# Optimization experiments

Hardware: AMD Instinct MI355X
Metric: run time of the kernel (lower is better)

The kernel has to match this reference:

```python
import jax, jax.numpy as jnp
import numpy as np

N = 50000      # nodes
E = 800000     # edges
D_IN = 128
D_H = 128      # dim_h
D_OUT = 1
G = 64         # graphs in batch


def _glorot(key, fan_in, fan_out):
    return jax.random.normal(key, (fan_in, fan_out), jnp.float32) / np.sqrt(fan_in)


def setup_inputs() -> dict:
    key = jax.random.key(0)
    ks = jax.random.split(key, 12)
    x = jax.random.normal(ks[0], (N, D_IN), jnp.float32)
    edge_index = jax.random.randint(ks[1], (2, E), 0, N, dtype=jnp.int32)
    batch = jnp.sort(jax.random.randint(ks[2], (N,), 0, G, dtype=jnp.int32))
    # SAGEConv params: lin_l (bias) on aggregated neighbors, lin_r (no bias) on root
    Wl1 = _glorot(ks[3], D_IN, 2 * D_H); bl1 = jnp.zeros((2 * D_H,), jnp.float32)
    Wr1 = _glorot(ks[4], D_IN, 2 * D_H)
    Wl2 = _glorot(ks[5], 2 * D_H, D_H); bl2 = jnp.zeros((D_H,), jnp.float32)
    Wr2 = _glorot(ks[6], 2 * D_H, D_H)
    Wl3 = _glorot(ks[7], D_H, 16); bl3 = jnp.zeros((16,), jnp.float32)
    Wr3 = _glorot(ks[8], D_H, 16)
    Wc = _glorot(ks[9], 16, D_OUT); bc = jnp.zeros((D_OUT,), jnp.float32)
    return dict(x=x, edge_index=edge_index, batch=batch,
                Wl1=Wl1, bl1=bl1, Wr1=Wr1,
                Wl2=Wl2, bl2=bl2, Wr2=Wr2,
                Wl3=Wl3, bl3=bl3, Wr3=Wr3,
                Wc=Wc, bc=bc)


def _segment_mean(vals, ids, num_segments):
    s = jax.ops.segment_sum(vals, ids, num_segments=num_segments)
    cnt = jax.ops.segment_sum(jnp.ones((vals.shape[0], 1), vals.dtype), ids,
                              num_segments=num_segments)
    return s / jnp.maximum(cnt, 1.0)


def _sage_conv(x, src, dst, Wl, bl, Wr):
    # PyG SAGEConv (mean aggr): lin_l(mean_{j in N(i)} x_j) + lin_r(x_i)
    mean_nbr = _segment_mean(x[src], dst, x.shape[0])  # gather + segment-mean
    return mean_nbr @ Wl + bl + x @ Wr


def reference(x, edge_index, batch,
              Wl1, bl1, Wr1, Wl2, bl2, Wr2, Wl3, bl3, Wr3, Wc, bc):
    src, dst = edge_index[0], edge_index[1]
    h = jax.nn.relu(_sage_conv(x, src, dst, Wl1, bl1, Wr1))   # [N, 256]
    # dropout p=0.5 skipped (training=False)
    h = jax.nn.relu(_sage_conv(h, src, dst, Wl2, bl2, Wr2))   # [N, 128]
    # dropout p=0.2 skipped (training=False)
    h = _sage_conv(h, src, dst, Wl3, bl3, Wr3)                # [N, 16]
    h_pool = _segment_mean(h, batch, G)                       # global_mean_pool [G,16]
    # final dropout is hardcoded training=True in source -> fixed-key dropout
    keep = jax.random.bernoulli(jax.random.key(42), 0.5, h_pool.shape)
    hd = jnp.where(keep, h_pool * 2.0, 0.0)
    out = (hd @ Wc + bc).reshape(-1)                          # [G*dim_out]
    return out, h_pool
```

## Files before the change

kernel.cpp:

```cpp
#include <hip/hip_runtime.h>
#include <stdint.h>


#define GG 64
#define NXCD 8
#define BCAP 112000

typedef __attribute__((ext_vector_type(8))) unsigned short ushort8;
typedef __attribute__((ext_vector_type(8))) short bf16s8;
typedef __attribute__((ext_vector_type(4))) float f32x4;

__device__ __forceinline__ unsigned short rne_bf16(float f) {
  unsigned u = __float_as_uint(f);
  return (unsigned short)((u + 0x7FFFu + ((u >> 16) & 1u)) >> 16);
}
__device__ __forceinline__ float bf2f(unsigned short b) {
  return __uint_as_float(((unsigned)b) << 16);
}

__global__ __launch_bounds__(256) void k_cvtprep(const float* __restrict__ x, unsigned short* __restrict__ xb,
                                                 int n8, int N,
                                                 const float* __restrict__ Wl1, const float* __restrict__ Wr1,
                                                 const float* __restrict__ Wl2, const float* __restrict__ Wr2,
                                                 const float* __restrict__ Wl3, const float* __restrict__ Wr3,
                                                 unsigned short* __restrict__ WT1l, unsigned short* __restrict__ WT1r,
                                                 unsigned short* __restrict__ WT2l, unsigned short* __restrict__ WT2r,
                                                 unsigned short* __restrict__ wc3b,
                                                 int* __restrict__ deg, int* __restrict__ bcur) {
  int idx = blockIdx.x * 256 + threadIdx.x;
  if (idx < n8) {
    const float4* p = (const float4*)(x + (size_t)idx * 8);
    float4 v0 = p[0], v1 = p[1];
    ushort8 o;
    o[0] = rne_bf16(v0.x); o[1] = rne_bf16(v0.y); o[2] = rne_bf16(v0.z); o[3] = rne_bf16(v0.w);
    o[4] = rne_bf16(v1.x); o[5] = rne_bf16(v1.y); o[6] = rne_bf16(v1.z); o[7] = rne_bf16(v1.w);
    *(ushort8*)(xb + (size_t)idx * 8) = o;
    return;
  }
  int j = idx - n8;
  if (j < 32768) {
    int k = j >> 8, m = j & 255;
    WT1l[m * 128 + k] = rne_bf16(Wl1[j]);
    WT1r[m * 128 + k] = rne_bf16(Wr1[j]);
  } else if (j < 65536) {
    int q = j - 32768;
    int k = q >> 7, m = q & 127;
    WT2l[m * 256 + k] = rne_bf16(Wl2[q]);
    WT2r[m * 256 + k] = rne_bf16(Wr2[q]);
  } else if (j < 69632) {
    int q = j - 65536;
    int m = q >> 7, k = q & 127;
    float v = (m < 16) ? Wl3[k * 16 + m] : Wr3[k * 16 + (m - 16)];
    wc3b[q] = rne_bf16(v);
  } else if (j < 69632 + N) {
    deg[j - 69632] = 0;
  } else if (j < 69632 + N + NXCD) {
    bcur[j - 69632 - N] = 0;
  }
}

__global__ __launch_bounds__(256) void k_bucket(const int* __restrict__ src, const int* __restrict__ dst,
                                                int* __restrict__ deg, int* __restrict__ bcur,
                                                int2* __restrict__ bucket, int E, int binsz) {
  __shared__ int cnt[NXCD];
  __shared__ int base[NXCD];
  const int tid = threadIdx.x;
  if (tid < NXCD) cnt[tid] = 0;
  __syncthreads();
  int e0 = (blockIdx.x * 256 + tid) * 4;
  int d[4], s[4], bk[4], rk[4];
  int nv = 0;
  if (e0 + 3 < E) {
    int4 d4 = *(const int4*)(dst + e0);
    int4 s4 = *(const int4*)(src + e0);
    d[0] = d4.x; d[1] = d4.y; d[2] = d4.z; d[3] = d4.w;
    s[0] = s4.x; s[1] = s4.y; s[2] = s4.z; s[3] = s4.w;
    nv = 4;
  } else {
    for (int e = e0; e < E && nv < 4; ++e) { d[nv] = dst[e]; s[nv] = src[e]; ++nv; }
  }
#pragma unroll
  for (int k = 0; k < 4; ++k)
    if (k < nv) {
      atomicAdd(&deg[d[k]], 1);
      bk[k] = d[k] / binsz;
      rk[k] = atomicAdd(&cnt[bk[k]], 1);
    }
  __syncthreads();
  if (tid < NXCD) base[tid] = atomicAdd(&bcur[tid], cnt[tid]);
  __syncthreads();
#pragma unroll
  for (int k = 0; k < 4; ++k)
    if (k < nv) {
      int p = min(base[bk[k]] + rk[k], BCAP - 1);
      bucket[(size_t)bk[k] * BCAP + p] = make_int2(s[k], d[k]);
    }
}

__global__ __launch_bounds__(256) void k_scan_a(const int* __restrict__ deg, int* __restrict__ off,
                                                int* __restrict__ bsum, int N) {
  __shared__ int ws[256];
  const int tid = threadIdx.x;
  const int base = blockIdx.x * 1024 + tid * 4;
  int v0 = (base + 0 < N) ? deg[base + 0] : 0;
  int v1 = (base + 1 < N) ? deg[base + 1] : 0;
  int v2 = (base + 2 < N) ? deg[base + 2] : 0;
  int v3 = (base + 3 < N) ? deg[base + 3] : 0;
  int s = v0 + v1 + v2 + v3;
  ws[tid] = s;
  __syncthreads();
  for (int d = 1; d < 256; d <<= 1) {
    int t = (tid >= d) ? ws[tid - d] : 0;
    __syncthreads();
    ws[tid] += t;
    __syncthreads();
  }
  int excl = ws[tid] - s;
  if (tid == 255) bsum[blockIdx.x] = ws[255];
  if (base + 0 < N) off[base + 0] = excl;
  if (base + 1 < N) off[base + 1] = excl + v0;
  if (base + 2 < N) off[base + 2] = excl + v0 + v1;
  if (base + 3 < N) off[base + 3] = excl + v0 + v1 + v2;
}

__global__ __launch_bounds__(64) void k_scan_b(int* __restrict__ bsum, int nb) {
  int tid = threadIdx.x;
  int v = (tid < nb) ? bsum[tid] : 0;
  for (int d = 1; d < 64; d <<= 1) {
    int t = __shfl_up(v, d, 64);
    if (tid >= d) v += t;
  }
  if (tid < nb) bsum[tid] = v;
}

__global__ __launch_bounds__(256) void k_scan_c(int* __restrict__ off, int* __restrict__ cur,
                                                const int* __restrict__ bsum, int N, int nb) {
  int i = blockIdx.x * 256 + threadIdx.x;
  if (i < N) {
    int b = i >> 10;
    int v = off[i] + ((b > 0) ? bsum[b - 1] : 0);
    off[i] = v;
    cur[i] = v;
  }
  if (i == 0) off[N] = bsum[nb - 1];
}

__global__ __launch_bounds__(256) void k_fill2(const int2* __restrict__ bucket, const int* __restrict__ bcnt,
                                               const int* __restrict__ off, int* __restrict__ cur,
                                               int* __restrict__ eidx, int N, int binsz, int ngrp) {
  const int xcd = blockIdx.x & (NXCD - 1);
  const int grp = blockIdx.x >> 3;
  const int t = grp * 256 + threadIdx.x;
  const int nthr = ngrp * 256;
  const int lo = xcd * binsz;
  const int hi = min(lo + binsz, N);

  int s0 = off[lo] & ~15;
  int s1 = off[hi];
  for (int i = s0 + t * 16; i < s1; i += nthr * 16) {
    int v = eidx[i];
    asm volatile("" :: "v"(v));
  }

  const int cnt = min(bcnt[xcd], BCAP);
  const int2* seg = bucket + (size_t)xcd * BCAP;
  for (int e = t; e < cnt; e += nthr) {
    int2 sd = seg[e];
    int p = atomicAdd(&cur[sd.y], 1);
    eidx[p] = sd.x;
  }
}

template <int OUTBF>
__global__ __launch_bounds__(256) void k_aggr_b(const unsigned short* __restrict__ feat,
                                                const int* __restrict__ off, const int* __restrict__ eidx,
                                                void* __restrict__ out, int N) {
  int idx = blockIdx.x * 256 + threadIdx.x;
  int n = idx >> 4;
  if (n >= N) return;
  int c = (idx & 15) * 8;
  int b = off[n], e = off[n + 1];
  float s0 = 0.f, s1 = 0.f, s2 = 0.f, s3 = 0.f, s4 = 0.f, s5 = 0.f, s6 = 0.f, s7 = 0.f;
  int j = b;
  for (; j + 3 < e; j += 4) {
    int i0 = eidx[j], i1 = eidx[j + 1], i2 = eidx[j + 2], i3 = eidx[j + 3];
    ushort8 v0 = *(const ushort8*)&feat[(size_t)i0 * 128 + c];
    ushort8 v1 = *(const ushort8*)&feat[(size_t)i1 * 128 + c];
    ushort8 v2 = *(const ushort8*)&feat[(size_t)i2 * 128 + c];
    ushort8 v3 = *(const ushort8*)&feat[(size_t)i3 * 128 + c];
    s0 += bf2f(v0[0]) + bf2f(v1[0]) + bf2f(v2[0]) + bf2f(v3[0]);
    s1 += bf2f(v0[1]) + bf2f(v1[1]) + bf2f(v2[1]) + bf2f(v3[1]);
    s2 += bf2f(v0[2]) + bf2f(v1[2]) + bf2f(v2[2]) + bf2f(v3[2]);
    s3 += bf2f(v0[3]) + bf2f(v1[3]) + bf2f(v2[3]) + bf2f(v3[3]);
    s4 += bf2f(v0[4]) + bf2f(v1[4]) + bf2f(v2[4]) + bf2f(v3[4]);
    s5 += bf2f(v0[5]) + bf2f(v1[5]) + bf2f(v2[5]) + bf2f(v3[5]);
    s6 += bf2f(v0[6]) + bf2f(v1[6]) + bf2f(v2[6]) + bf2f(v3[6]);
    s7 += bf2f(v0[7]) + bf2f(v1[7]) + bf2f(v2[7]) + bf2f(v3[7]);
  }
  for (; j < e; ++j) {
    int sidx = eidx[j];
    ushort8 v = *(const ushort8*)&feat[(size_t)sidx * 128 + c];
    s0 += bf2f(v[0]); s1 += bf2f(v[1]); s2 += bf2f(v[2]); s3 += bf2f(v[3]);
    s4 += bf2f(v[4]); s5 += bf2f(v[5]); s6 += bf2f(v[6]); s7 += bf2f(v[7]);
  }
  float sc = 1.f / fmaxf((float)(e - b), 1.f);
  if (OUTBF) {
    ushort8 o;
    o[0] = rne_bf16(s0 * sc); o[1] = rne_bf16(s1 * sc); o[2] = rne_bf16(s2 * sc); o[3] = rne_bf16(s3 * sc);
    o[4] = rne_bf16(s4 * sc); o[5] = rne_bf16(s5 * sc); o[6] = rne_bf16(s6 * sc); o[7] = rne_bf16(s7 * sc);
    *(ushort8*)&((unsigned short*)out)[(size_t)n * 128 + c] = o;
  } else {
    float* po = &((float*)out)[(size_t)n * 128 + c];
    *(float4*)po = make_float4(s0 * sc, s1 * sc, s2 * sc, s3 * sc);
    *(float4*)(po + 4) = make_float4(s4 * sc, s5 * sc, s6 * sc, s7 * sc);
  }
}

template <int DUAL, int HAS_C0, int HAS_BIAS, int RELU, int OUT_BF16>
__global__ __launch_bounds__(256) void k_mgemm(
    const unsigned short* __restrict__ A1, int K1, const unsigned short* __restrict__ B1,
    const unsigned short* __restrict__ A2, const unsigned short* __restrict__ B2, int K2,
    const float* __restrict__ C0, const float* __restrict__ bias,
    void* __restrict__ Cout, int N, int M) {
  __shared__ unsigned short As[64 * 32];
  __shared__ unsigned short Bs[64 * 32];
  const int tid = threadIdx.x;
  const int row0 = blockIdx.y * 64;
  const int col0 = blockIdx.x * 64;
  const int lane = tid & 63;
  const int w = tid >> 6;
  const int wr = w >> 1, wc = w & 1;
  const int rl = lane & 15, g = lane >> 4;
  const int pos = ((g ^ ((rl >> 1) & 3)) << 3);
  const int srow = tid >> 2;
  const int schunk = tid & 3;
  const int spos = ((schunk ^ ((srow >> 1) & 3)) << 3);

  f32x4 acc00 = {0.f, 0.f, 0.f, 0.f}, acc01 = acc00, acc10 = acc00, acc11 = acc00;

  for (int pass = 0; pass < (DUAL ? 2 : 1); ++pass) {
    const unsigned short* __restrict__ A = pass ? A2 : A1;
    const unsigned short* __restrict__ B = pass ? B2 : B1;
    const int K = pass ? K2 : K1;
    for (int k0 = 0; k0 < K; k0 += 32) {
      {
        int r = row0 + srow;
        ushort8 va = (ushort8)(0);
        if (r < N) va = *(const ushort8*)&A[(size_t)r * K + k0 + schunk * 8];
        *(ushort8*)&As[srow * 32 + spos] = va;
        ushort8 vb = *(const ushort8*)&B[(size_t)(col0 + srow) * K + k0 + schunk * 8];
        *(ushort8*)&Bs[srow * 32 + spos] = vb;
      }
      __syncthreads();
      bf16s8 a0 = *(bf16s8*)&As[(wr * 32 + rl) * 32 + pos];
      bf16s8 a1 = *(bf16s8*)&As[(wr * 32 + 16 + rl) * 32 + pos];
      bf16s8 b0 = *(bf16s8*)&Bs[(wc * 32 + rl) * 32 + pos];
      bf16s8 b1 = *(bf16s8*)&Bs[(wc * 32 + 16 + rl) * 32 + pos];
      acc00 = __builtin_amdgcn_mfma_f32_16x16x32_bf16(a0, b0, acc00, 0, 0, 0);
      acc01 = __builtin_amdgcn_mfma_f32_16x16x32_bf16(a0, b1, acc01, 0, 0, 0);
      acc10 = __builtin_amdgcn_mfma_f32_16x16x32_bf16(a1, b0, acc10, 0, 0, 0);
      acc11 = __builtin_amdgcn_mfma_f32_16x16x32_bf16(a1, b1, acc11, 0, 0, 0);
      __syncthreads();
    }
  }

#pragma unroll
  for (int fi = 0; fi < 2; ++fi)
#pragma unroll
    for (int fj = 0; fj < 2; ++fj) {
      const f32x4 a = fi ? (fj ? acc11 : acc10) : (fj ? acc01 : acc00);
#pragma unroll
      for (int reg = 0; reg < 4; ++reg) {
        int r = row0 + wr * 32 + fi * 16 + g * 4 + reg;
        int c = col0 + wc * 32 + fj * 16 + rl;
        if (r >= N) continue;
        float v = a[reg];
        if (HAS_C0) v += C0[(size_t)r * M + c];
        if (HAS_BIAS) v += bias[c];
        if (RELU) v = fmaxf(v, 0.f);
        if (OUT_BF16) ((unsigned short*)Cout)[(size_t)r * M + c] = rne_bf16(v);
        else ((float*)Cout)[(size_t)r * M + c] = v;
      }
    }
}

__global__ __launch_bounds__(256) void k_mgemm3(const unsigned short* __restrict__ A,
                                                const unsigned short* __restrict__ B,
                                                float* __restrict__ C, int N) {
  __shared__ unsigned short As[128 * 32];
  __shared__ unsigned short Bs[32 * 32];
  const int tid = threadIdx.x;
  const int row0 = blockIdx.x * 128;
  const int lane = tid & 63;
  const int w = tid >> 6;
  const int rl = lane & 15, g = lane >> 4;
  const int pos = ((g ^ ((rl >> 1) & 3)) << 3);

  f32x4 acc00 = {0.f, 0.f, 0.f, 0.f}, acc01 = acc00, acc10 = acc00, acc11 = acc00;

  for (int k0 = 0; k0 < 128; k0 += 32) {
#pragma unroll
    for (int it = 0; it < 2; ++it) {
      int cid = tid + it * 256;
      int row = cid >> 2, ch = cid & 3;
      int r = row0 + row;
      ushort8 va = (ushort8)(0);
      if (r < N) va = *(const ushort8*)&A[(size_t)r * 128 + k0 + ch * 8];
      *(ushort8*)&As[row * 32 + ((ch ^ ((row >> 1) & 3)) << 3)] = va;
    }
    if (tid < 128) {
      int row = tid >> 2, ch = tid & 3;
      ushort8 vb = *(const ushort8*)&B[(size_t)row * 128 + k0 + ch * 8];
      *(ushort8*)&Bs[row * 32 + ((ch ^ ((row >> 1) & 3)) << 3)] = vb;
    }
    __syncthreads();
    bf16s8 a0 = *(bf16s8*)&As[(w * 32 + rl) * 32 + pos];
    bf16s8 a1 = *(bf16s8*)&As[(w * 32 + 16 + rl) * 32 + pos];
    bf16s8 b0 = *(bf16s8*)&Bs[rl * 32 + pos];
    bf16s8 b1 = *(bf16s8*)&Bs[(16 + rl) * 32 + pos];
    acc00 = __builtin_amdgcn_mfma_f32_16x16x32_bf16(a0, b0, acc00, 0, 0, 0);
    acc01 = __builtin_amdgcn_mfma_f32_16x16x32_bf16(a0, b1, acc01, 0, 0, 0);
    acc10 = __builtin_amdgcn_mfma_f32_16x16x32_bf16(a1, b0, acc10, 0, 0, 0);
    acc11 = __builtin_amdgcn_mfma_f32_16x16x32_bf16(a1, b1, acc11, 0, 0, 0);
    __syncthreads();
  }

#pragma unroll
  for (int fi = 0; fi < 2; ++fi)
#pragma unroll
    for (int fj = 0; fj < 2; ++fj) {
      const f32x4 a = fi ? (fj ? acc11 : acc10) : (fj ? acc01 : acc00);
#pragma unroll
      for (int reg = 0; reg < 4; ++reg) {
        int r = row0 + w * 32 + fi * 16 + g * 4 + reg;
        int c = fj * 16 + rl;
        if (r < N) C[(size_t)r * 32 + c] = a[reg];
      }
    }
}

__global__ __launch_bounds__(256) void k_l3post(const float* __restrict__ g3, const int* __restrict__ off,
                                                const int* __restrict__ eidx, const float* __restrict__ bl3,
                                                float* __restrict__ h3, int N) {
  int idx = blockIdx.x * 256 + threadIdx.x;
  int n = idx >> 2;
  if (n >= N) return;
  int c = (idx & 3) << 2;
  int b = off[n], e = off[n + 1];
  float ax = 0.f, ay = 0.f, az = 0.f, aw = 0.f;
  int j = b;
  for (; j + 3 < e; j += 4) {
    int i0 = eidx[j], i1 = eidx[j + 1], i2 = eidx[j + 2], i3 = eidx[j + 3];
    const float4 v0 = *(const float4*)&g3[(size_t)i0 * 32 + c];
    const float4 v1 = *(const float4*)&g3[(size_t)i1 * 32 + c];
    const float4 v2 = *(const float4*)&g3[(size_t)i2 * 32 + c];
    const float4 v3 = *(const float4*)&g3[(size_t)i3 * 32 + c];
    ax += v0.x + v1.x + v2.x + v3.x;
    ay += v0.y + v1.y + v2.y + v3.y;
    az += v0.z + v1.z + v2.z + v3.z;
    aw += v0.w + v1.w + v2.w + v3.w;
  }
  for (; j < e; ++j) {
    int s = eidx[j];
    const float4 v = *(const float4*)&g3[(size_t)s * 32 + c];
    ax += v.x; ay += v.y; az += v.z; aw += v.w;
  }
  float sc = 1.f / fmaxf((float)(e - b), 1.f);
  const float4 r2 = *(const float4*)&g3[(size_t)n * 32 + 16 + c];
  const float4 bb = *(const float4*)&bl3[c];
  *(float4*)&h3[(size_t)n * 16 + c] =
      make_float4(ax * sc + r2.x + bb.x, ay * sc + r2.y + bb.y,
                  az * sc + r2.z + bb.z, aw * sc + r2.w + bb.w);
}

__device__ __forceinline__ int lbound(const int* __restrict__ a, int n, int v) {
  int lo = 0, hi = n;
  while (lo < hi) {
    int mid = (lo + hi) >> 1;
    if (a[mid] < v) lo = mid + 1; else hi = mid;
  }
  return lo;
}

__global__ __launch_bounds__(256) void k_pool(const float* __restrict__ h3, const int* __restrict__ batch,
                                              int N, float* __restrict__ hpool, float* __restrict__ outp) {
  __shared__ float sm[4][16];
  int g = blockIdx.x, tid = threadIdx.x;
  int start = lbound(batch, N, g);
  int end = lbound(batch, N, g + 1);
  float acc[16];
#pragma unroll
  for (int j = 0; j < 16; ++j) acc[j] = 0.f;
  for (int i = start + tid; i < end; i += 256) {
    const float4* p = (const float4*)&h3[(size_t)i * 16];
    float4 v0 = p[0], v1 = p[1], v2 = p[2], v3 = p[3];
    acc[0] += v0.x; acc[1] += v0.y; acc[2] += v0.z; acc[3] += v0.w;
    acc[4] += v1.x; acc[5] += v1.y; acc[6] += v1.z; acc[7] += v1.w;
    acc[8] += v2.x; acc[9] += v2.y; acc[10] += v2.z; acc[11] += v2.w;
    acc[12] += v3.x; acc[13] += v3.y; acc[14] += v3.z; acc[15] += v3.w;
  }
#pragma unroll
  for (int j = 0; j < 16; ++j) {
    float v = acc[j];
    v += __shfl_down(v, 32);
    v += __shfl_down(v, 16);
    v += __shfl_down(v, 8);
    v += __shfl_down(v, 4);
    v += __shfl_down(v, 2);
    v += __shfl_down(v, 1);
    if ((tid & 63) == 0) sm[tid >> 6][j] = v;
  }
  __syncthreads();
  if (tid < 16) {
    float v = sm[0][tid] + sm[1][tid] + sm[2][tid] + sm[3][tid];
    v /= fmaxf((float)(end - start), 1.f);
    hpool[g * 16 + tid] = v;
    outp[g * 16 + tid] = v;
  }
}

__device__ __forceinline__ uint2 tf2x32(unsigned k0, unsigned k1, unsigned x0, unsigned x1) {
  const unsigned ks[3] = {k0, k1, k0 ^ k1 ^ 0x1BD11BDAu};
  const int rotA[4] = {13, 15, 26, 6}, rotB[4] = {17, 29, 16, 24};
  x0 += ks[0];
  x1 += ks[1];
#pragma unroll
  for (int i = 0; i < 5; ++i) {
    const int* R = (i & 1) ? rotB : rotA;
#pragma unroll
    for (int j = 0; j < 4; ++j) {
      x0 += x1;
      x1 = (x1 << R[j]) | (x1 >> (32 - R[j]));
      x1 ^= x0;
    }
    x0 += ks[(i + 1) % 3];
    x1 += ks[(i + 2) % 3] + (unsigned)(i + 1);
  }
  return make_uint2(x0, x1);
}

__global__ __launch_bounds__(1024) void k_final(const float* __restrict__ hpool,
                                                float* __restrict__ outp,
                                                const float* __restrict__ Wc,
                                                const float* __restrict__ bc) {
  int t = threadIdx.x;
  float m = hpool[t];
  uint2 r = tf2x32(0u, 42u, 0u, (unsigned)t);
  unsigned bits = r.x ^ r.y;
  float hd = (bits >> 31) ? 0.f : 2.f * m;
  float contrib = hd * Wc[t & 15];
  contrib += __shfl_down(contrib, 8, 16);
  contrib += __shfl_down(contrib, 4, 16);
  contrib += __shfl_down(contrib, 2, 16);
  contrib += __shfl_down(contrib, 1, 16);
  if ((t & 15) == 0) outp[t >> 4] = contrib + bc[0];
}

extern "C" void kernel_launch(void* const* d_in, const int* in_sizes, int n_in,
                              void* d_out, int out_size, void* d_ws, size_t ws_size,
                              hipStream_t stream) {
  const float* x   = (const float*)d_in[0];
  const int*   ei  = (const int*)d_in[1];
  const int*   bat = (const int*)d_in[2];
  const float* Wl1 = (const float*)d_in[3];
  const float* bl1 = (const float*)d_in[4];
  const float* Wr1 = (const float*)d_in[5];
  const float* Wl2 = (const float*)d_in[6];
  const float* bl2 = (const float*)d_in[7];
  const float* Wr2 = (const float*)d_in[8];
  const float* Wl3 = (const float*)d_in[9];
  const float* bl3 = (const float*)d_in[10];
  const float* Wr3 = (const float*)d_in[11];
  const float* Wc  = (const float*)d_in[12];
  const float* bc  = (const float*)d_in[13];

  const int E = in_sizes[1] / 2;
  const int N = in_sizes[2];
  const int* src = ei;
  const int* dst = ei + E;

  int*   off   = (int*)d_ws;
  int*   deg   = off + 50016;
  int*   bsum  = (int*)d_ws + 100016;
  int*   bcur  = (int*)d_ws + 100080;
  float* hpool = (float*)d_ws + 100096;
  unsigned short* wc3b = (unsigned short*)((float*)d_ws + 101120);
  unsigned short* WT1l = (unsigned short*)((float*)d_ws + 105216);
  unsigned short* WT1r = (unsigned short*)((float*)d_ws + 121600);
  unsigned short* WT2l = (unsigned short*)((float*)d_ws + 137984);
  unsigned short* WT2r = (unsigned short*)((float*)d_ws + 154368);
  int*   eidx  = (int*)d_ws + 170752;
  unsigned short* xb   = (unsigned short*)((float*)d_ws + 970752);
  unsigned short* aggb = (unsigned short*)((float*)d_ws + 4170752);
  unsigned short* h1b  = (unsigned short*)((float*)d_ws + 7370752);
  unsigned short* t2b  = xb;
  unsigned short* h2b  = (unsigned short*)((float*)d_ws + 970752);
  float* agg2 = (float*)d_ws + 13770752;
  int*   cur  = (int*)agg2;
  int2*  bucket = (int2*)((float*)d_ws + 13820800);
  float* g3   = (float*)d_ws + 7370752;
  float* h3   = (float*)d_ws + 8970752;
  float* outp = (float*)d_out;

  const int gy = (N + 63) / 64;
  const int gy3 = (N + 127) / 128;
  const int nb = (N + 1023) / 1024;
  const int n8 = N * 128 / 8;
  const int binsz = (N + NXCD - 1) / NXCD;
  const int ngrp = 64;

  const int prep_total = n8 + 69632 + N + NXCD;
  k_cvtprep<<<(prep_total + 255) / 256, 256, 0, stream>>>(x, xb, n8, N, Wl1, Wr1, Wl2, Wr2, Wl3, Wr3,
                                                          WT1l, WT1r, WT2l, WT2r, wc3b, deg, bcur);

  k_bucket<<<((E + 3) / 4 + 255) / 256, 256, 0, stream>>>(src, dst, deg, bcur, bucket, E, binsz);
  k_scan_a<<<nb, 256, 0, stream>>>(deg, off, bsum, N);
  k_scan_b<<<1, 64, 0, stream>>>(bsum, nb);
  k_scan_c<<<(N + 255) / 256, 256, 0, stream>>>(off, cur, bsum, N, nb);
  k_fill2<<<ngrp * NXCD, 256, 0, stream>>>(bucket, bcur, off, cur, eidx, N, binsz, ngrp);

  k_aggr_b<1><<<(N * 16 + 255) / 256, 256, 0, stream>>>(xb, off, eidx, aggb, N);
  k_mgemm<1, 0, 1, 1, 1><<<dim3(4, gy), 256, 0, stream>>>(aggb, 128, WT1l, xb, WT1r, 128,
                                                          nullptr, bl1, h1b, N, 256);

  k_mgemm<0, 0, 0, 0, 1><<<dim3(2, gy), 256, 0, stream>>>(h1b, 256, WT2l, nullptr, nullptr, 0,
                                                          nullptr, nullptr, t2b, N, 128);
  k_aggr_b<0><<<(N * 16 + 255) / 256, 256, 0, stream>>>(t2b, off, eidx, agg2, N);
  k_mgemm<0, 1, 1, 1, 1><<<dim3(2, gy), 256, 0, stream>>>(h1b, 256, WT2r, nullptr, nullptr, 0,
                                                          agg2, bl2, h2b, N, 128);

  k_mgemm3<<<gy3, 256, 0, stream>>>(h2b, wc3b, g3, N);
  k_l3post<<<(N * 4 + 255) / 256, 256, 0, stream>>>(g3, off, eidx, bl3, h3, N);

  k_pool<<<GG, 256, 0, stream>>>(h3, bat, N, hpool, outp + 64);
  k_final<<<1, 1024, 0, stream>>>(hpool, outp, Wc, bc);
}
```

Measured before the change: 241.8 us.

## Merge scan kernels, store layer-2 aggregate in bf16, fuse pool with final head

Replaces the three-kernel prefix scan with a single-block 1024-thread sequential-chunk scan. The layer-2 neighbour aggregate is now written as bf16 into the existing aggb buffer instead of fp32, halving that intermediate's traffic in both the aggregation and the GEMM epilogue. The pool and dropout/classifier kernels are fused into one, dropping a launch. Risks: the single-block scan walks about 49 chunks serially with many barriers, and bf16 rounding of the aggregate slightly reduces precision.

```diff
diff --git a/kernel.cpp b/kernel.cpp
--- a/kernel.cpp
+++ b/kernel.cpp
@@ -97,52 +97,32 @@
     }
 }
 
-__global__ __launch_bounds__(256) void k_scan_a(const int* __restrict__ deg, int* __restrict__ off,
-                                                int* __restrict__ bsum, int N) {
-  __shared__ int ws[256];
+__global__ __launch_bounds__(1024) void k_scan(const int* __restrict__ deg, int* __restrict__ off,
+                                               int* __restrict__ cur, int N) {
+  __shared__ int sm[1024];
   const int tid = threadIdx.x;
-  const int base = blockIdx.x * 1024 + tid * 4;
-  int v0 = (base + 0 < N) ? deg[base + 0] : 0;
-  int v1 = (base + 1 < N) ? deg[base + 1] : 0;
-  int v2 = (base + 2 < N) ? deg[base + 2] : 0;
-  int v3 = (base + 3 < N) ? deg[base + 3] : 0;
-  int s = v0 + v1 + v2 + v3;
-  ws[tid] = s;
-  __syncthreads();
-  for (int d = 1; d < 256; d <<= 1) {
-    int t = (tid >= d) ? ws[tid - d] : 0;
+  int running = 0;
+  for (int base = 0; base < N; base += 1024) {
+    int i = base + tid;
+    int v = (i < N) ? deg[i] : 0;
+    sm[tid] = v;
     __syncthreads();
-    ws[tid] += t;
+    for (int d = 1; d < 1024; d <<= 1) {
+      int t = (tid >= d) ? sm[tid - d] : 0;
+      __syncthreads();
+      sm[tid] += t;
+      __syncthreads();
+    }
+    if (i < N) {
+      int o = running + sm[tid] - v;
+      off[i] = o;
+      cur[i] = o;
+    }
+    int ct = sm[1023];
     __syncthreads();
-  }
-  int excl = ws[tid] - s;
-  if (tid == 255) bsum[blockIdx.x] = ws[255];
-  if (base + 0 < N) off[base + 0] = excl;
-  if (base + 1 < N) off[base + 1] = excl + v0;
-  if (base + 2 < N) off[base + 2] = excl + v0 + v1;
-  if (base + 3 < N) off[base + 3] = excl + v0 + v1 + v2;
-}
-
-__global__ __launch_bounds__(64) void k_scan_b(int* __restrict__ bsum, int nb) {
-  int tid = threadIdx.x;
-  int v = (tid < nb) ? bsum[tid] : 0;
-  for (int d = 1; d < 64; d <<= 1) {
-    int t = __shfl_up(v, d, 64);
-    if (tid >= d) v += t;
-  }
-  if (tid < nb) bsum[tid] = v;
-}
-
-__global__ __launch_bounds__(256) void k_scan_c(int* __restrict__ off, int* __restrict__ cur,
-                                                const int* __restrict__ bsum, int N, int nb) {
-  int i = blockIdx.x * 256 + threadIdx.x;
-  if (i < N) {
-    int b = i >> 10;
-    int v = off[i] + ((b > 0) ? bsum[b - 1] : 0);
-    off[i] = v;
-    cur[i] = v;
-  }
-  if (i == 0) off[N] = bsum[nb - 1];
+    running += ct;
+  }
+  if (tid == 0) off[N] = running;
 }
 
 __global__ __launch_bounds__(256) void k_fill2(const int2* __restrict__ bucket, const int* __restrict__ bcnt,
@@ -171,10 +151,9 @@
   }
 }
 
-template <int OUTBF>
 __global__ __launch_bounds__(256) void k_aggr_b(const unsigned short* __restrict__ feat,
                                                 const int* __restrict__ off, const int* __restrict__ eidx,
-                                                void* __restrict__ out, int N) {
+                                                unsigned short* __restrict__ out, int N) {
   int idx = blockIdx.x * 256 + threadIdx.x;
   int n = idx >> 4;
   if (n >= N) return;
@@ -204,23 +183,17 @@
     s4 += bf2f(v[4]); s5 += bf2f(v[5]); s6 += bf2f(v[6]); s7 += bf2f(v[7]);
   }
   float sc = 1.f / fmaxf((float)(e - b), 1.f);
-  if (OUTBF) {
-    ushort8 o;
-    o[0] = rne_bf16(s0 * sc); o[1] = rne_bf16(s1 * sc); o[2] = rne_bf16(s2 * sc); o[3] = rne_bf16(s3 * sc);
-    o[4] = rne_bf16(s4 * sc); o[5] = rne_bf16(s5 * sc); o[6] = rne_bf16(s6 * sc); o[7] = rne_bf16(s7 * sc);
-    *(ushort8*)&((unsigned short*)out)[(size_t)n * 128 + c] = o;
-  } else {
-    float* po = &((float*)out)[(size_t)n * 128 + c];
-    *(float4*)po = make_float4(s0 * sc, s1 * sc, s2 * sc, s3 * sc);
-    *(float4*)(po + 4) = make_float4(s4 * sc, s5 * sc, s6 * sc, s7 * sc);
-  }
+  ushort8 o;
+  o[0] = rne_bf16(s0 * sc); o[1] = rne_bf16(s1 * sc); o[2] = rne_bf16(s2 * sc); o[3] = rne_bf16(s3 * sc);
+  o[4] = rne_bf16(s4 * sc); o[5] = rne_bf16(s5 * sc); o[6] = rne_bf16(s6 * sc); o[7] = rne_bf16(s7 * sc);
+  *(ushort8*)&out[(size_t)n * 128 + c] = o;
 }
 
 template <int DUAL, int HAS_C0, int HAS_BIAS, int RELU, int OUT_BF16>
 __global__ __launch_bounds__(256) void k_mgemm(
     const unsigned short* __restrict__ A1, int K1, const unsigned short* __restrict__ B1,
     const unsigned short* __restrict__ A2, const unsigned short* __restrict__ B2, int K2,
-    const float* __restrict__ C0, const float* __restrict__ bias,
+    const unsigned short* __restrict__ C0, const float* __restrict__ bias,
     void* __restrict__ Cout, int N, int M) {
   __shared__ unsigned short As[64 * 32];
   __shared__ unsigned short Bs[64 * 32];
@@ -275,7 +248,7 @@
         int c = col0 + wc * 32 + fj * 16 + rl;
         if (r >= N) continue;
         float v = a[reg];
-        if (HAS_C0) v += C0[(size_t)r * M + c];
+        if (HAS_C0) v += bf2f(C0[(size_t)r * M + c]);
         if (HAS_BIAS) v += bias[c];
         if (RELU) v = fmaxf(v, 0.f);
         if (OUT_BF16) ((unsigned short*)Cout)[(size_t)r * M + c] = rne_bf16(v);
@@ -373,6 +346,26 @@
                   az * sc + r2.z + bb.z, aw * sc + r2.w + bb.w);
 }
 
+__device__ __forceinline__ uint2 tf2x32(unsigned k0, unsigned k1, unsigned x0, unsigned x1) {
+  const unsigned ks[3] = {k0, k1, k0 ^ k1 ^ 0x1BD11BDAu};
+  const int rotA[4] = {13, 15, 26, 6}, rotB[4] = {17, 29, 16, 24};
+  x0 += ks[0];
+  x1 += ks[1];
+#pragma unroll
+  for (int i = 0; i < 5; ++i) {
+    const int* R = (i & 1) ? rotB : rotA;
+#pragma unroll
+    for (int j = 0; j < 4; ++j) {
+      x0 += x1;
+      x1 = (x1 << R[j]) | (x1 >> (32 - R[j]));
+      x1 ^= x0;
+    }
+    x0 += ks[(i + 1) % 3];
+    x1 += ks[(i + 2) % 3] + (unsigned)(i + 1);
+  }
+  return make_uint2(x0, x1);
+}
+
 __device__ __forceinline__ int lbound(const int* __restrict__ a, int n, int v) {
   int lo = 0, hi = n;
   while (lo < hi) {
@@ -382,8 +375,9 @@
   return lo;
 }
 
-__global__ __launch_bounds__(256) void k_pool(const float* __restrict__ h3, const int* __restrict__ batch,
-                                              int N, float* __restrict__ hpool, float* __restrict__ outp) {
+__global__ __launch_bounds__(256) void k_poolfinal(const float* __restrict__ h3, const int* __restrict__ batch,
+                                                   int N, const float* __restrict__ Wc,
+                                                   const float* __restrict__ bc, float* __restrict__ outp) {
   __shared__ float sm[4][16];
   int g = blockIdx.x, tid = threadIdx.x;
   int start = lbound(batch, N, g);
@@ -414,46 +408,17 @@
   if (tid < 16) {
     float v = sm[0][tid] + sm[1][tid] + sm[2][tid] + sm[3][tid];
     v /= fmaxf((float)(end - start), 1.f);
-    hpool[g * 16 + tid] = v;
-    outp[g * 16 + tid] = v;
-  }
-}
-
-__device__ __forceinline__ uint2 tf2x32(unsigned k0, unsigned k1, unsigned x0, unsigned x1) {
-  const unsigned ks[3] = {k0, k1, k0 ^ k1 ^ 0x1BD11BDAu};
-  const int rotA[4] = {13, 15, 26, 6}, rotB[4] = {17, 29, 16, 24};
-  x0 += ks[0];
-  x1 += ks[1];
-#pragma unroll
-  for (int i = 0; i < 5; ++i) {
-    const int* R = (i & 1) ? rotB : rotA;
-#pragma unroll
-    for (int j = 0; j < 4; ++j) {
-      x0 += x1;
-      x1 = (x1 << R[j]) | (x1 >> (32 - R[j]));
-      x1 ^= x0;
-    }
-    x0 += ks[(i + 1) % 3];
-    x1 += ks[(i + 2) % 3] + (unsigned)(i + 1);
-  }
-  return make_uint2(x0, x1);
-}
-
-__global__ __launch_bounds__(1024) void k_final(const float* __restrict__ hpool,
-                                                float* __restrict__ outp,
-                                                const float* __restrict__ Wc,
-                                                const float* __restrict__ bc) {
-  int t = threadIdx.x;
-  float m = hpool[t];
-  uint2 r = tf2x32(0u, 42u, 0u, (unsigned)t);
-  unsigned bits = r.x ^ r.y;
-  float hd = (bits >> 31) ? 0.f : 2.f * m;
-  float contrib = hd * Wc[t & 15];
-  contrib += __shfl_down(contrib, 8, 16);
-  contrib += __shfl_down(contrib, 4, 16);
-  contrib += __shfl_down(contrib, 2, 16);
-  contrib += __shfl_down(contrib, 1, 16);
-  if ((t & 15) == 0) outp[t >> 4] = contrib + bc[0];
+    outp[64 + g * 16 + tid] = v;
+    uint2 r = tf2x32(0u, 42u, 0u, (unsigned)(g * 16 + tid));
+    unsigned bits = r.x ^ r.y;
+    float hd = (bits >> 31) ? 0.f : 2.f * v;
+    float contrib = hd * Wc[tid];
+    contrib += __shfl_down(contrib, 8, 16);
+    contrib += __shfl_down(contrib, 4, 16);
+    contrib += __shfl_down(contrib, 2, 16);
+    contrib += __shfl_down(contrib, 1, 16);
+    if (tid == 0) outp[g] = contrib + bc[0];
+  }
 }
 
 extern "C" void kernel_launch(void* const* d_in, const int* in_sizes, int n_in,
@@ -481,9 +446,7 @@
 
   int*   off   = (int*)d_ws;
   int*   deg   = off + 50016;
-  int*   bsum  = (int*)d_ws + 100016;
   int*   bcur  = (int*)d_ws + 100080;
-  float* hpool = (float*)d_ws + 100096;
   unsigned short* wc3b = (unsigned short*)((float*)d_ws + 101120);
   unsigned short* WT1l = (unsigned short*)((float*)d_ws + 105216);
   unsigned short* WT1r = (unsigned short*)((float*)d_ws + 121600);
@@ -495,8 +458,7 @@
   unsigned short* h1b  = (unsigned short*)((float*)d_ws + 7370752);
   unsigned short* t2b  = xb;
   unsigned short* h2b  = (unsigned short*)((float*)d_ws + 970752);
-  float* agg2 = (float*)d_ws + 13770752;
-  int*   cur  = (int*)agg2;
+  int*   cur  = (int*)((float*)d_ws + 13770752);
   int2*  bucket = (int2*)((float*)d_ws + 13820800);
   float* g3   = (float*)d_ws + 7370752;
   float* h3   = (float*)d_ws + 8970752;
@@ -504,7 +466,6 @@
 
   const int gy = (N + 63) / 64;
   const int gy3 = (N + 127) / 128;
-  const int nb = (N + 1023) / 1024;
   const int n8 = N * 128 / 8;
   const int binsz = (N + NXCD - 1) / NXCD;
   const int ngrp = 64;
@@ -514,24 +475,21 @@
                                                           WT1l, WT1r, WT2l, WT2r, wc3b, deg, bcur);
 
   k_bucket<<<((E + 3) / 4 + 255) / 256, 256, 0, stream>>>(src, dst, deg, bcur, bucket, E, binsz);
-  k_scan_a<<<nb, 256, 0, stream>>>(deg, off, bsum, N);
-  k_scan_b<<<1, 64, 0, stream>>>(bsum, nb);
-  k_scan_c<<<(N + 255) / 256, 256, 0, stream>>>(off, cur, bsum, N, nb);
+  k_scan<<<1, 1024, 0, stream>>>(deg, off, cur, N);
   k_fill2<<<ngrp * NXCD, 256, 0, stream>>>(bucket, bcur, off, cur, eidx, N, binsz, ngrp);
 
-  k_aggr_b<1><<<(N * 16 + 255) / 256, 256, 0, stream>>>(xb, off, eidx, aggb, N);
+  k_aggr_b<<<(N * 16 + 255) / 256, 256, 0, stream>>>(xb, off, eidx, aggb, N);
   k_mgemm<1, 0, 1, 1, 1><<<dim3(4, gy), 256, 0, stream>>>(aggb, 128, WT1l, xb, WT1r, 128,
                                                           nullptr, bl1, h1b, N, 256);
 
   k_mgemm<0, 0, 0, 0, 1><<<dim3(2, gy), 256, 0, stream>>>(h1b, 256, WT2l, nullptr, nullptr, 0,
                                                           nullptr, nullptr, t2b, N, 128);
-  k_aggr_b<0><<<(N * 16 + 255) / 256, 256, 0, stream>>>(t2b, off, eidx, agg2, N);
+  k_aggr_b<<<(N * 16 + 255) / 256, 256, 0, stream>>>(t2b, off, eidx, aggb, N);
   k_mgemm<0, 1, 1, 1, 1><<<dim3(2, gy), 256, 0, stream>>>(h1b, 256, WT2r, nullptr, nullptr, 0,
-                                                          agg2, bl2, h2b, N, 128);
+                                                          aggb, bl2, h2b, N, 128);
 
   k_mgemm3<<<gy3, 256, 0, stream>>>(h2b, wc3b, g3, N);
   k_l3post<<<(N * 4 + 255) / 256, 256, 0, stream>>>(g3, off, eidx, bl3, h3, N);
 
-  k_pool<<<GG, 256, 0, stream>>>(h3, bat, N, hpool, outp + 64);
-  k_final<<<1, 1024, 0, stream>>>(hpool, outp, Wc, bc);
-}
+  k_poolfinal<<<GG, 256, 0, stream>>>(h3, bat, N, Wc, bc, outp);
+}
```

New measurement: 318.2 us. 31.6% more time.
